# Optimization experiments

Measured on AMD Instinct MI355X. Metric: run time of the kernel, lower is better.

The kernel has to match this reference:

```python
import jax, jax.numpy as jnp
import numpy as np

B, S, HID = 1, 2048, 4096
H, KV, D = 32, 8, 128          # query heads, kv heads, head_dim
THETA = 100000.0               # rope base


def setup_inputs() -> dict:
    key = jax.random.key(0)
    k1, k2, k3, k4, k5 = jax.random.split(key, 5)
    hidden_states = jax.random.normal(k1, (B, S, HID), jnp.float32)
    # W_pack: Linear(hidden, H*D + 2*KV*D), torch weight layout [out, in]
    w_pack = jax.random.normal(k2, (H * D + 2 * KV * D, HID), jnp.float32) * 0.02
    w_o = jax.random.normal(k3, (HID, H * D), jnp.float32) * 0.02
    # conv kernels: per-kv-head causal mixing weights of width 2 (softmax-normalized at init)
    conv_k = jax.nn.softmax(jax.random.normal(k4, (KV, 2), jnp.float32), axis=-1)
    conv_v = jax.nn.softmax(jax.random.normal(k5, (KV, 2), jnp.float32), axis=-1)
    return dict(hidden_states=hidden_states, w_pack=w_pack, w_o=w_o,
                conv_k=conv_k, conv_v=conv_v)


def _causal_conv2(u, k):
    """u: [b,s,h,d], k: [h,2]. v[t] = k[h,0]*u[t-1] + k[h,1]*u[t] (zero pad at t=-1).
    Equivalent to custom_convolution with window 2 (unfold+mul+sum)."""
    prev = jnp.pad(u, ((0, 0), (1, 0), (0, 0), (0, 0)))[:, :-1]
    return k[None, None, :, 0:1] * prev + k[None, None, :, 1:2] * u


def _rope(x):
    """Non-interleaved (half-split) rotary over full head_dim. x: [b,s,h,d]."""
    s, d = x.shape[1], x.shape[-1]
    inv = 1.0 / (THETA ** (jnp.arange(0, d, 2, dtype=jnp.float32) / d))
    freqs = jnp.arange(s, dtype=jnp.float32)[:, None] * inv[None, :]  # [s, d/2]
    cos = jnp.cos(freqs)[None, :, None, :]
    sin = jnp.sin(freqs)[None, :, None, :]
    x1, x2 = x[..., : d // 2], x[..., d // 2:]
    return jnp.concatenate([x1 * cos - x2 * sin, x1 * sin + x2 * cos], axis=-1)


def reference(hidden_states, w_pack, w_o, conv_k, conv_v):
    qkv = hidden_states @ w_pack.T                       # [b,s,H*D+2*KV*D]
    q = qkv[..., : H * D].reshape(B, S, H, D)
    k = qkv[..., H * D: H * D + KV * D].reshape(B, S, KV, D)
    v = qkv[..., H * D + KV * D:].reshape(B, S, KV, D)

    # causal depthwise width-2 conv mixing on K and V (prefill path)
    k = _causal_conv2(k, conv_k)
    v = _causal_conv2(v, conv_v)

    # rotary on q, k
    q = _rope(q)
    k = _rope(k)

    # GQA: repeat kv heads to match query heads
    g = H // KV
    k = jnp.repeat(k, g, axis=2)
    v = jnp.repeat(v, g, axis=2)

    scale = 1.0 / np.sqrt(D).astype(np.float32)
    scores = jnp.einsum('bqhd,bkhd->bhqk', q, k) * scale  # [b,H,S,S]
    causal = jnp.tril(jnp.ones((S, S), dtype=bool))
    scores = jnp.where(causal[None, None], scores, jnp.finfo(scores.dtype).min)
    probs = jax.nn.softmax(scores, axis=-1)
    out = jnp.einsum('bhqk,bkhd->bqhd', probs, v).reshape(B, S, H * D)
    return out @ w_o.T
```

## Files before the change

### kernel.cpp

```cpp
#include <hip/hip_runtime.h>
#include <hip/hip_bf16.h>

#define S_LEN 2048
#define HID 4096
#define NH 32
#define NKV 8
#define HD 128

typedef unsigned short u16;
typedef __attribute__((ext_vector_type(4))) float f32x4;
typedef __attribute__((ext_vector_type(8))) short bf16x8;

__device__ __forceinline__ u16 f2bf(float x) {
  union { float f; unsigned u; } c; c.f = x;
  unsigned r = c.u + 0x7FFFu + ((c.u >> 16) & 1u);
  return (u16)(r >> 16);
}

__device__ __forceinline__ void gload16(const void* g, void* l) {
  __builtin_amdgcn_global_load_lds(
      (const __attribute__((address_space(1))) unsigned int*)g,
      (__attribute__((address_space(3))) unsigned int*)l, 16, 0, 0);
}

__global__ void cvt4_kernel(const float* __restrict__ s, u16* __restrict__ d, int n4) {
  int i = blockIdx.x * 256 + threadIdx.x;
  if (i >= n4) return;
  float4 v = ((const float4*)s)[i];
  ushort4 o;
  o.x = f2bf(v.x); o.y = f2bf(v.y); o.z = f2bf(v.z); o.w = f2bf(v.w);
  ((ushort4*)d)[i] = o;
}

__global__ void rope_tab_kernel(float2* __restrict__ tab) {
  int i = blockIdx.x * 256 + threadIdx.x;
  int t = i >> 6, d = i & 63;
  float inv = expf(-(float)d * (11.512925464970229f / 64.0f));
  float f = (float)t * inv;
  float2 cs; cs.x = cosf(f); cs.y = sinf(f);
  tab[i] = cs;
}

__global__ void rope_q_kernel(const float* __restrict__ qkv, const float2* __restrict__ tab,
                              u16* __restrict__ Q) {
  int i = blockIdx.x * 256 + threadIdx.x;
  int d = i & 63, h = (i >> 6) & 31, t = i >> 11;
  const float* row = qkv + (size_t)t * 6144 + h * 128;
  float x1 = row[d], x2 = row[d + 64];
  float2 cs = tab[(t << 6) | d];
  const float SC = 0.12752551286084f;
  u16* orow = Q + (((size_t)t * NH + h) << 7);
  orow[d]      = f2bf((x1 * cs.x - x2 * cs.y) * SC);
  orow[d + 64] = f2bf((x1 * cs.y + x2 * cs.x) * SC);
}

__global__ void convrope_k_kernel(const float* __restrict__ qkv, const float* __restrict__ ck,
                                  const float2* __restrict__ tab, u16* __restrict__ K) {
  int i = blockIdx.x * 256 + threadIdx.x;
  int d = i & 63, kv = (i >> 6) & 7, t = i >> 9;
  const float* cur = qkv + (size_t)t * 6144 + 4096 + kv * 128;
  float c0 = ck[kv * 2], c1 = ck[kv * 2 + 1];
  float x1 = c1 * cur[d], x2 = c1 * cur[d + 64];
  if (t > 0) { const float* prv = cur - 6144; x1 += c0 * prv[d]; x2 += c0 * prv[d + 64]; }
  float2 cs = tab[(t << 6) | d];
  u16* orow = K + (((size_t)t * NKV + kv) << 7);
  orow[d]      = f2bf(x1 * cs.x - x2 * cs.y);
  orow[d + 64] = f2bf(x1 * cs.y + x2 * cs.x);
}

__global__ __launch_bounds__(256) void convT_v_kernel(const float* __restrict__ qkv,
                                                      const float* __restrict__ cv,
                                                      u16* __restrict__ VT) {
  __shared__ float ld[65][128];
  int tt = blockIdx.x * 64, kv = blockIdx.y;
  float c0 = cv[kv * 2], c1 = cv[kv * 2 + 1];
  for (int idx = threadIdx.x; idx < 65 * 128; idx += 256) {
    int r = idx >> 7, d = idx & 127;
    int t = tt - 1 + r;
    ld[r][d] = (t >= 0) ? qkv[(size_t)t * 6144 + 5120 + kv * 128 + d] : 0.f;
  }
  __syncthreads();
  int d = threadIdx.x >> 1, tc = (threadIdx.x & 1) * 32;
  u16* out = VT + ((size_t)kv * 128 + d) * S_LEN + tt + tc;
#pragma unroll
  for (int j = 0; j < 32; ++j)
    out[j] = f2bf(c0 * ld[tc + j][d] + c1 * ld[tc + j + 1][d]);
}

#define BM 128
#define BN 128
#define BK 64

__global__ __launch_bounds__(256, 2) void gemm_nt_kernel(const u16* __restrict__ A,
                                                         const u16* __restrict__ B,
                                                         float* __restrict__ C,
                                                         int M, int N, int K) {
  __shared__ __align__(16) u16 lA[BM * BK];
  __shared__ __align__(16) u16 lB[BN * BK];
  const int tid = threadIdx.x;
  const int wid = tid >> 6, lane = tid & 63;
  const int bm = blockIdx.y * BM, bn = blockIdx.x * BN;
  const int wr = (wid >> 1) * 64, wc = (wid & 1) * 64;
  const int lr = lane & 15, lg = lane >> 4;
  f32x4 acc[4][4] = {};
  const char* Ab = (const char*)A;
  const char* Bb = (const char*)B;
  const int nk = K / BK;
  for (int kt = 0; kt < nk; ++kt) {
    const size_t k0b = (size_t)kt * (BK * 2);
    __syncthreads();
#pragma unroll
    for (int i = 0; i < 4; ++i) {
      int off = (i * 4 + wid) * 1024 + lane * 16;
      int row = off >> 7, inrow = off & 127;
      int sw = inrow ^ ((row & 7) << 4);
      gload16(Ab + (size_t)(bm + row) * (K * 2) + k0b + sw, (char*)lA + (i * 4 + wid) * 1024);
      gload16(Bb + (size_t)(bn + row) * (K * 2) + k0b + sw, (char*)lB + (i * 4 + wid) * 1024);
    }
    __syncthreads();
    bf16x8 af[4][2], bfv[4][2];
#pragma unroll
    for (int m = 0; m < 4; ++m)
#pragma unroll
      for (int ks = 0; ks < 2; ++ks) {
        int row = wr + m * 16 + lr;
        int boff = row * 128 + ((ks * 64 + lg * 16) ^ ((row & 7) << 4));
        af[m][ks] = *(const bf16x8*)((const char*)lA + boff);
      }
#pragma unroll
    for (int n = 0; n < 4; ++n)
#pragma unroll
      for (int ks = 0; ks < 2; ++ks) {
        int row = wc + n * 16 + lr;
        int boff = row * 128 + ((ks * 64 + lg * 16) ^ ((row & 7) << 4));
        bfv[n][ks] = *(const bf16x8*)((const char*)lB + boff);
      }
#pragma unroll
    for (int m = 0; m < 4; ++m)
#pragma unroll
      for (int n = 0; n < 4; ++n)
#pragma unroll
        for (int ks = 0; ks < 2; ++ks)
          acc[m][n] = __builtin_amdgcn_mfma_f32_16x16x32_bf16(af[m][ks], bfv[n][ks], acc[m][n], 0, 0, 0);
  }
#pragma unroll
  for (int m = 0; m < 4; ++m)
#pragma unroll
    for (int n = 0; n < 4; ++n)
#pragma unroll
      for (int r = 0; r < 4; ++r) {
        int row = bm + wr + m * 16 + lg * 4 + r;
        int col = bn + wc + n * 16 + lr;
        C[(size_t)row * N + col] = acc[m][n][r];
      }
}

__global__ __launch_bounds__(256, 2) void attn_kernel(const u16* __restrict__ Q,
                                                      const u16* __restrict__ K,
                                                      const u16* __restrict__ VT,
                                                      u16* __restrict__ O) {
  __shared__ __align__(16) u16 lK[2][64 * 128];
  __shared__ __align__(16) u16 lV[2][128 * 64];
  __shared__ __align__(16) u16 lP[4][16 * 64];
  const int tid = threadIdx.x;
  const int wid = tid >> 6, lane = tid & 63;
  const int lr = lane & 15, lg = lane >> 4;
  const int q0 = blockIdx.x, h = blockIdx.y;
  const int kvh = h >> 2;
  const int qtA = q0, qtB = 31 - q0;

  bf16x8 qfA[4], qfB[4];
  {
    const int rA = qtA * 64 + wid * 16 + lr;
    const int rB = qtB * 64 + wid * 16 + lr;
#pragma unroll
    for (int ks = 0; ks < 4; ++ks) {
      qfA[ks] = *(const bf16x8*)(Q + (((size_t)rA * NH + h) << 7) + ks * 32 + lg * 8);
      qfB[ks] = *(const bf16x8*)(Q + (((size_t)rB * NH + h) << 7) + ks * 32 + lg * 8);
    }
  }

  f32x4 oA[8] = {}, oB[8] = {};
  float mA[4], lsA[4], mB[4], lsB[4];
#pragma unroll
  for (int r = 0; r < 4; ++r) { mA[r] = mB[r] = -1e30f; lsA[r] = lsB[r] = 0.f; }

  const char* Kb = (const char*)K;
  const char* Vb = (const char*)VT;
  char* pb = (char*)lP[wid];

  auto stage = [&](int buf, int kt) {
    char* dK = (char*)lK[buf];
    char* dV = (char*)lV[buf];
#pragma unroll
    for (int i = 0; i < 4; ++i) {
      int off = (i * 4 + wid) * 1024 + lane * 16;
      int t = off >> 8, inrow = off & 255;
      gload16(Kb + (((size_t)((kt * 64 + t) * NKV + kvh)) << 8) + (inrow ^ ((t & 7) << 4)),
              dK + (i * 4 + wid) * 1024);
      int d = off >> 7, inr2 = off & 127;
      gload16(Vb + ((size_t)(kvh * 128 + d)) * (S_LEN * 2) + kt * 128 + (inr2 ^ ((d & 7) << 4)),
              dV + (i * 4 + wid) * 1024);
    }
  };

  auto step = [&](const bf16x8* qf, f32x4* o, float* mrow, float* lrow, int buf, bool diag) {
    const char* kb = (const char*)lK[buf];
    const char* vb = (const char*)lV[buf];
    f32x4 sv[4];
#pragma unroll
    for (int n = 0; n < 4; ++n) {
      f32x4 a = {};
#pragma unroll
      for (int ks = 0; ks < 4; ++ks) {
        int trow = n * 16 + lr;
        int boff = trow * 256 + ((ks * 64 + lg * 16) ^ ((trow & 7) << 4));
        bf16x8 kf = *(const bf16x8*)(kb + boff);
        a = __builtin_amdgcn_mfma_f32_16x16x32_bf16(qf[ks], kf, a, 0, 0, 0);
      }
      sv[n] = a;
    }
    if (diag) {
#pragma unroll
      for (int n = 0; n < 4; ++n)
#pragma unroll
        for (int r = 0; r < 4; ++r) {
          int col = n * 16 + lr, rw = wid * 16 + lg * 4 + r;
          if (col > rw) sv[n][r] = -1e30f;
        }
    }
    float pm[4];
#pragma unroll
    for (int r = 0; r < 4; ++r)
      pm[r] = fmaxf(fmaxf(sv[0][r], sv[1][r]), fmaxf(sv[2][r], sv[3][r]));
#pragma unroll
    for (int r = 0; r < 4; ++r) {
      pm[r] = fmaxf(pm[r], __shfl_xor(pm[r], 1));
      pm[r] = fmaxf(pm[r], __shfl_xor(pm[r], 2));
      pm[r] = fmaxf(pm[r], __shfl_xor(pm[r], 4));
      pm[r] = fmaxf(pm[r], __shfl_xor(pm[r], 8));
    }
    bool need = (pm[0] > mrow[0] + 8.f) | (pm[1] > mrow[1] + 8.f) |
                (pm[2] > mrow[2] + 8.f) | (pm[3] > mrow[3] + 8.f);
    if (__any(need)) {
#pragma unroll
      for (int r = 0; r < 4; ++r) {
        float mn = fmaxf(mrow[r], pm[r]);
        float al = exp2f(mrow[r] - mn);
        mrow[r] = mn;
        lrow[r] *= al;
#pragma unroll
        for (int nt = 0; nt < 8; ++nt) o[nt][r] *= al;
      }
    }
    float rs[4] = {0.f, 0.f, 0.f, 0.f};
#pragma unroll
    for (int n = 0; n < 4; ++n)
#pragma unroll
      for (int r = 0; r < 4; ++r) {
        float p = exp2f(sv[n][r] - mrow[r]);
        rs[r] += p;
        int row = lg * 4 + r, col = n * 16 + lr;
        int boff = (row * 128 + col * 2) ^ ((row & 7) << 4);
        *(u16*)(pb + boff) = f2bf(p);
      }
#pragma unroll
    for (int r = 0; r < 4; ++r) {
      rs[r] += __shfl_xor(rs[r], 1);
      rs[r] += __shfl_xor(rs[r], 2);
      rs[r] += __shfl_xor(rs[r], 4);
      rs[r] += __shfl_xor(rs[r], 8);
      lrow[r] += rs[r];
    }
#pragma unroll
    for (int ks = 0; ks < 2; ++ks) {
      int aboff = lr * 128 + ((ks * 64 + lg * 16) ^ ((lr & 7) << 4));
      bf16x8 pf = *(const bf16x8*)(pb + aboff);
#pragma unroll
      for (int nt = 0; nt < 8; ++nt) {
        int drow = nt * 16 + lr;
        int vboff = drow * 128 + ((ks * 64 + lg * 16) ^ ((drow & 7) << 4));
        bf16x8 vf = *(const bf16x8*)(vb + vboff);
        o[nt] = __builtin_amdgcn_mfma_f32_16x16x32_bf16(pf, vf, o[nt], 0, 0, 0);
      }
    }
  };

  stage(0, 0);
  __syncthreads();
  for (int kt = 0; kt <= qtB; ++kt) {
    int cur = kt & 1;
    if (kt < qtB) stage(cur ^ 1, kt + 1);
    if (kt <= qtA) step(qfA, oA, mA, lsA, cur, kt == qtA);
    step(qfB, oB, mB, lsB, cur, kt == qtB);
    __syncthreads();
  }

#pragma unroll
  for (int r = 0; r < 4; ++r) { lsA[r] = 1.0f / lsA[r]; lsB[r] = 1.0f / lsB[r]; }
#pragma unroll
  for (int nt = 0; nt < 8; ++nt)
#pragma unroll
    for (int r = 0; r < 4; ++r) {
      int rowA = qtA * 64 + wid * 16 + lg * 4 + r;
      int rowB = qtB * 64 + wid * 16 + lg * 4 + r;
      int col = nt * 16 + lr;
      O[(size_t)rowA * 4096 + h * 128 + col] = f2bf(oA[nt][r] * lsA[r]);
      O[(size_t)rowB * 4096 + h * 128 + col] = f2bf(oB[nt][r] * lsB[r]);
    }
}

extern "C" void kernel_launch(void* const* d_in, const int* in_sizes, int n_in,
                              void* d_out, int out_size, void* d_ws, size_t ws_size,
                              hipStream_t stream) {
  const float* hidden = (const float*)d_in[0];
  const float* wpack  = (const float*)d_in[1];
  const float* wo     = (const float*)d_in[2];
  const float* convk  = (const float*)d_in[3];
  const float* convv  = (const float*)d_in[4];
  float* out = (float*)d_out;

  char* w = (char*)d_ws;
  u16*  hiddenB = (u16*)w;
  u16*  wpackB  = (u16*)(w + 16777216);
  float* qkv    = (float*)(w + 67108864);
  u16*  qrope   = (u16*)(w + 117440512);
  u16*  krope   = (u16*)(w + 134217728);
  u16*  vT      = (u16*)(w + 138412032);
  float2* tab   = (float2*)(w + 142606336);

  cvt4_kernel<<<8192, 256, 0, stream>>>(hidden, hiddenB, 2097152);
  cvt4_kernel<<<24576, 256, 0, stream>>>(wpack, wpackB, 6291456);
  rope_tab_kernel<<<512, 256, 0, stream>>>(tab);
  gemm_nt_kernel<<<dim3(48, 16), 256, 0, stream>>>(hiddenB, wpackB, qkv, 2048, 6144, 4096);
  cvt4_kernel<<<16384, 256, 0, stream>>>(wo, wpackB, 4194304);
  rope_q_kernel<<<16384, 256, 0, stream>>>(qkv, tab, qrope);
  convrope_k_kernel<<<4096, 256, 0, stream>>>(qkv, convk, tab, krope);
  convT_v_kernel<<<dim3(32, 8), 256, 0, stream>>>(qkv, convv, vT);
  attn_kernel<<<dim3(16, 32), 256, 0, stream>>>(qrope, krope, vT, hiddenB);
  gemm_nt_kernel<<<dim3(32, 16), 256, 0, stream>>>(hiddenB, wpackB, out, 2048, 4096, 4096);
}
```

Before: 530.2 us.

## Split attention q-tiles across wave pairs and remap GEMM blocks per XCD

In the attention kernel, each wave used to process 16 rows of both the low and high q-tile. Now two waves own the low tile and two own the high tile, 32 rows each. This shares each K/V fragment load across two MFMAs and removes the serialized A and B steps per wave. The GEMM kernel also remaps block IDs so consecutive tiles land on the same XCD for better L2 locality. The cost is load imbalance: waves on the short tile sit idle while the long tile finishes, and the larger P buffer raises LDS use and register pressure.

```diff
diff --git a/kernel.cpp b/kernel.cpp
--- a/kernel.cpp
+++ b/kernel.cpp
@@ -99,7 +99,11 @@
   __shared__ __align__(16) u16 lB[BN * BK];
   const int tid = threadIdx.x;
   const int wid = tid >> 6, lane = tid & 63;
-  const int bm = blockIdx.y * BM, bn = blockIdx.x * BN;
+  const int nbx = gridDim.x, nwg = nbx * gridDim.y;
+  const int L = blockIdx.y * nbx + blockIdx.x;
+  const int cpx = nwg >> 3;
+  const int W = (L & 7) * cpx + (L >> 3);
+  const int bm = (W / nbx) * BM, bn = (W % nbx) * BN;
   const int wr = (wid >> 1) * 64, wc = (wid & 1) * 64;
   const int lr = lane & 15, lg = lane >> 4;
   f32x4 acc[4][4] = {};
@@ -161,29 +165,30 @@
                                                       u16* __restrict__ O) {
   __shared__ __align__(16) u16 lK[2][64 * 128];
   __shared__ __align__(16) u16 lV[2][128 * 64];
-  __shared__ __align__(16) u16 lP[4][16 * 64];
+  __shared__ __align__(16) u16 lP[4][32 * 64];
   const int tid = threadIdx.x;
   const int wid = tid >> 6, lane = tid & 63;
   const int lr = lane & 15, lg = lane >> 4;
   const int q0 = blockIdx.x, h = blockIdx.y;
   const int kvh = h >> 2;
   const int qtA = q0, qtB = 31 - q0;
-
-  bf16x8 qfA[4], qfB[4];
-  {
-    const int rA = qtA * 64 + wid * 16 + lr;
-    const int rB = qtB * 64 + wid * 16 + lr;
-#pragma unroll
-    for (int ks = 0; ks < 4; ++ks) {
-      qfA[ks] = *(const bf16x8*)(Q + (((size_t)rA * NH + h) << 7) + ks * 32 + lg * 8);
-      qfB[ks] = *(const bf16x8*)(Q + (((size_t)rB * NH + h) << 7) + ks * 32 + lg * 8);
-    }
-  }
-
-  f32x4 oA[8] = {}, oB[8] = {};
-  float mA[4], lsA[4], mB[4], lsB[4];
-#pragma unroll
-  for (int r = 0; r < 4; ++r) { mA[r] = mB[r] = -1e30f; lsA[r] = lsB[r] = 0.f; }
+  const int tile = wid >> 1, w2 = wid & 1;
+  const int qt = tile ? qtB : qtA;
+  const int qbase = qt * 64 + w2 * 32;
+
+  bf16x8 qf[2][4];
+#pragma unroll
+  for (int m = 0; m < 2; ++m)
+#pragma unroll
+    for (int ks = 0; ks < 4; ++ks)
+      qf[m][ks] = *(const bf16x8*)(Q + (((size_t)(qbase + m * 16 + lr) * NH + h) << 7) + ks * 32 + lg * 8);
+
+  f32x4 o[2][8] = {};
+  float mrow[2][4], lrow[2][4];
+#pragma unroll
+  for (int m = 0; m < 2; ++m)
+#pragma unroll
+    for (int r = 0; r < 4; ++r) { mrow[m][r] = -1e30f; lrow[m][r] = 0.f; }
 
   const char* Kb = (const char*)K;
   const char* Vb = (const char*)VT;
@@ -204,84 +209,101 @@
     }
   };
 
-  auto step = [&](const bf16x8* qf, f32x4* o, float* mrow, float* lrow, int buf, bool diag) {
+  auto step = [&](int buf, bool diag) {
     const char* kb = (const char*)lK[buf];
     const char* vb = (const char*)lV[buf];
-    f32x4 sv[4];
-#pragma unroll
-    for (int n = 0; n < 4; ++n) {
-      f32x4 a = {};
+    f32x4 sv[2][4] = {};
+#pragma unroll
+    for (int n = 0; n < 4; ++n)
 #pragma unroll
       for (int ks = 0; ks < 4; ++ks) {
         int trow = n * 16 + lr;
         int boff = trow * 256 + ((ks * 64 + lg * 16) ^ ((trow & 7) << 4));
         bf16x8 kf = *(const bf16x8*)(kb + boff);
-        a = __builtin_amdgcn_mfma_f32_16x16x32_bf16(qf[ks], kf, a, 0, 0, 0);
-      }
-      sv[n] = a;
-    }
+        sv[0][n] = __builtin_amdgcn_mfma_f32_16x16x32_bf16(qf[0][ks], kf, sv[0][n], 0, 0, 0);
+        sv[1][n] = __builtin_amdgcn_mfma_f32_16x16x32_bf16(qf[1][ks], kf, sv[1][n], 0, 0, 0);
+      }
     if (diag) {
 #pragma unroll
+      for (int m = 0; m < 2; ++m)
+#pragma unroll
+        for (int n = 0; n < 4; ++n)
+#pragma unroll
+          for (int r = 0; r < 4; ++r) {
+            int col = n * 16 + lr, rw = w2 * 32 + m * 16 + lg * 4 + r;
+            if (col > rw) sv[m][n][r] = -1e30f;
+          }
+    }
+    float pm[2][4];
+#pragma unroll
+    for (int m = 0; m < 2; ++m)
+#pragma unroll
+      for (int r = 0; r < 4; ++r) {
+        float v = fmaxf(fmaxf(sv[m][0][r], sv[m][1][r]), fmaxf(sv[m][2][r], sv[m][3][r]));
+        v = fmaxf(v, __shfl_xor(v, 1));
+        v = fmaxf(v, __shfl_xor(v, 2));
+        v = fmaxf(v, __shfl_xor(v, 4));
+        v = fmaxf(v, __shfl_xor(v, 8));
+        pm[m][r] = v;
+      }
+    bool need = false;
+#pragma unroll
+    for (int m = 0; m < 2; ++m)
+#pragma unroll
+      for (int r = 0; r < 4; ++r)
+        need |= (pm[m][r] > mrow[m][r] + 8.f);
+    if (__any(need)) {
+#pragma unroll
+      for (int m = 0; m < 2; ++m)
+#pragma unroll
+        for (int r = 0; r < 4; ++r) {
+          float mn = fmaxf(mrow[m][r], pm[m][r]);
+          float al = exp2f(mrow[m][r] - mn);
+          mrow[m][r] = mn;
+          lrow[m][r] *= al;
+#pragma unroll
+          for (int nt = 0; nt < 8; ++nt) o[m][nt][r] *= al;
+        }
+    }
+#pragma unroll
+    for (int m = 0; m < 2; ++m) {
+      float rs[4] = {0.f, 0.f, 0.f, 0.f};
+#pragma unroll
       for (int n = 0; n < 4; ++n)
 #pragma unroll
         for (int r = 0; r < 4; ++r) {
-          int col = n * 16 + lr, rw = wid * 16 + lg * 4 + r;
-          if (col > rw) sv[n][r] = -1e30f;
+          float p = exp2f(sv[m][n][r] - mrow[m][r]);
+          rs[r] += p;
+          int row = m * 16 + lg * 4 + r, col = n * 16 + lr;
+          int boff = (row * 128 + col * 2) ^ ((row & 7) << 4);
+          *(u16*)(pb + boff) = f2bf(p);
         }
-    }
-    float pm[4];
-#pragma unroll
-    for (int r = 0; r < 4; ++r)
-      pm[r] = fmaxf(fmaxf(sv[0][r], sv[1][r]), fmaxf(sv[2][r], sv[3][r]));
-#pragma unroll
-    for (int r = 0; r < 4; ++r) {
-      pm[r] = fmaxf(pm[r], __shfl_xor(pm[r], 1));
-      pm[r] = fmaxf(pm[r], __shfl_xor(pm[r], 2));
-      pm[r] = fmaxf(pm[r], __shfl_xor(pm[r], 4));
-      pm[r] = fmaxf(pm[r], __shfl_xor(pm[r], 8));
-    }
-    bool need = (pm[0] > mrow[0] + 8.f) | (pm[1] > mrow[1] + 8.f) |
-                (pm[2] > mrow[2] + 8.f) | (pm[3] > mrow[3] + 8.f);
-    if (__any(need)) {
 #pragma unroll
       for (int r = 0; r < 4; ++r) {
-        float mn = fmaxf(mrow[r], pm[r]);
-        float al = exp2f(mrow[r] - mn);
-        mrow[r] = mn;
-        lrow[r] *= al;
-#pragma unroll
-        for (int nt = 0; nt < 8; ++nt) o[nt][r] *= al;
-      }
-    }
-    float rs[4] = {0.f, 0.f, 0.f, 0.f};
-#pragma unroll
-    for (int n = 0; n < 4; ++n)
-#pragma unroll
-      for (int r = 0; r < 4; ++r) {
-        float p = exp2f(sv[n][r] - mrow[r]);
-        rs[r] += p;
-        int row = lg * 4 + r, col = n * 16 + lr;
-        int boff = (row * 128 + col * 2) ^ ((row & 7) << 4);
-        *(u16*)(pb + boff) = f2bf(p);
-      }
-#pragma unroll
-    for (int r = 0; r < 4; ++r) {
-      rs[r] += __shfl_xor(rs[r], 1);
-      rs[r] += __shfl_xor(rs[r], 2);
-      rs[r] += __shfl_xor(rs[r], 4);
-      rs[r] += __shfl_xor(rs[r], 8);
-      lrow[r] += rs[r];
+        float v = rs[r];
+        v += __shfl_xor(v, 1);
+        v += __shfl_xor(v, 2);
+        v += __shfl_xor(v, 4);
+        v += __shfl_xor(v, 8);
+        lrow[m][r] += v;
+      }
     }
 #pragma unroll
     for (int ks = 0; ks < 2; ++ks) {
-      int aboff = lr * 128 + ((ks * 64 + lg * 16) ^ ((lr & 7) << 4));
-      bf16x8 pf = *(const bf16x8*)(pb + aboff);
+      bf16x8 pf[2];
+#pragma unroll
+      for (int m = 0; m < 2; ++m) {
+        int prow = m * 16 + lr;
+        int aboff = prow * 128 + ((ks * 64 + lg * 16) ^ ((prow & 7) << 4));
+        pf[m] = *(const bf16x8*)(pb + aboff);
+      }
 #pragma unroll
       for (int nt = 0; nt < 8; ++nt) {
         int drow = nt * 16 + lr;
         int vboff = drow * 128 + ((ks * 64 + lg * 16) ^ ((drow & 7) << 4));
         bf16x8 vf = *(const bf16x8*)(vb + vboff);
-        o[nt] = __builtin_amdgcn_mfma_f32_16x16x32_bf16(pf, vf, o[nt], 0, 0, 0);
+        o[0][nt] = __builtin_amdgcn_mfma_f32_16x16x32_bf16(pf[0], vf, o[0][nt], 0, 0, 0);
+        o[1][nt] = __builtin_amdgcn_mfma_f32_16x16x32_bf16(pf[1], vf, o[1][nt], 0, 0, 0);
       }
     }
   };
@@ -291,23 +313,24 @@
   for (int kt = 0; kt <= qtB; ++kt) {
     int cur = kt & 1;
     if (kt < qtB) stage(cur ^ 1, kt + 1);
-    if (kt <= qtA) step(qfA, oA, mA, lsA, cur, kt == qtA);
-    step(qfB, oB, mB, lsB, cur, kt == qtB);
+    if (kt <= qt) step(cur, kt == qt);
     __syncthreads();
   }
 
 #pragma unroll
-  for (int r = 0; r < 4; ++r) { lsA[r] = 1.0f / lsA[r]; lsB[r] = 1.0f / lsB[r]; }
-#pragma unroll
-  for (int nt = 0; nt < 8; ++nt)
-#pragma unroll
-    for (int r = 0; r < 4; ++r) {
-      int rowA = qtA * 64 + wid * 16 + lg * 4 + r;
-      int rowB = qtB * 64 + wid * 16 + lg * 4 + r;
-      int col = nt * 16 + lr;
-      O[(size_t)rowA * 4096 + h * 128 + col] = f2bf(oA[nt][r] * lsA[r]);
-      O[(size_t)rowB * 4096 + h * 128 + col] = f2bf(oB[nt][r] * lsB[r]);
-    }
+  for (int m = 0; m < 2; ++m)
+#pragma unroll
+    for (int r = 0; r < 4; ++r) lrow[m][r] = 1.0f / lrow[m][r];
+#pragma unroll
+  for (int m = 0; m < 2; ++m)
+#pragma unroll
+    for (int nt = 0; nt < 8; ++nt)
+#pragma unroll
+      for (int r = 0; r < 4; ++r) {
+        int row = qbase + m * 16 + lg * 4 + r;
+        int col = nt * 16 + lr;
+        O[(size_t)row * 4096 + h * 128 + col] = f2bf(o[m][nt][r] * lrow[m][r]);
+      }
 }
 
 extern "C" void kernel_launch(void* const* d_in, const int* in_sizes, int n_in,
```

New measurement: 555.0 us. 1.05x slower.

## Restructure attention to pair adjacent q-tiles, transpose QK^T, remap GEMM blocks across XCDs

Applied to the files above, without the earlier changes.

Each attention block now handles two adjacent query tiles (2b, 2b+1) instead of a head/tail pair. Work is ordered heaviest-first, and heads sharing a KV group are placed close together in the grid. QK^T is computed transposed so each lane owns one query row, which turns the row max and sum into two cross-lane shuffles. Packed bf16 conversion writes P to LDS, and the K/V fragment loads are shared between both tiles' MFMAs. GEMM workgroups are remapped so consecutive tiles land on the same XCD for L2 reuse. The cost is that paired adjacent tiles lose the balanced causal workload of the old head/tail pairing, and there are extra ds_bpermute broadcasts for rescaling.

```diff
diff --git a/kernel.cpp b/kernel.cpp
--- a/kernel.cpp
+++ b/kernel.cpp
@@ -21,6 +21,17 @@
   __builtin_amdgcn_global_load_lds(
       (const __attribute__((address_space(1))) unsigned int*)g,
       (__attribute__((address_space(3))) unsigned int*)l, 16, 0, 0);
+}
+
+__device__ __forceinline__ unsigned cvtpk_bf16(float lo, float hi) {
+  unsigned r;
+  asm("v_cvt_pk_bf16_f32 %0, %1, %2" : "=v"(r) : "v"(lo), "v"(hi));
+  return r;
+}
+
+__device__ __forceinline__ float bcastf(float v, int srclane) {
+  int r = __builtin_amdgcn_ds_bpermute(srclane << 2, __builtin_bit_cast(int, v));
+  return __builtin_bit_cast(float, r);
 }
 
 __global__ void cvt4_kernel(const float* __restrict__ s, u16* __restrict__ d, int n4) {
@@ -99,7 +110,11 @@
   __shared__ __align__(16) u16 lB[BN * BK];
   const int tid = threadIdx.x;
   const int wid = tid >> 6, lane = tid & 63;
-  const int bm = blockIdx.y * BM, bn = blockIdx.x * BN;
+  const int nbx = gridDim.x, nwg = nbx * gridDim.y;
+  const int L = blockIdx.y * nbx + blockIdx.x;
+  const int cpx = nwg >> 3;
+  const int W = (L & 7) * cpx + (L >> 3);
+  const int bm = (W / nbx) * BM, bn = (W % nbx) * BN;
   const int wr = (wid >> 1) * 64, wc = (wid & 1) * 64;
   const int lr = lane & 15, lg = lane >> 4;
   f32x4 acc[4][4] = {};
@@ -161,33 +176,33 @@
                                                       u16* __restrict__ O) {
   __shared__ __align__(16) u16 lK[2][64 * 128];
   __shared__ __align__(16) u16 lV[2][128 * 64];
-  __shared__ __align__(16) u16 lP[4][16 * 64];
+  __shared__ __align__(16) u16 lP[4][2][16 * 64];
   const int tid = threadIdx.x;
   const int wid = tid >> 6, lane = tid & 63;
   const int lr = lane & 15, lg = lane >> 4;
-  const int q0 = blockIdx.x, h = blockIdx.y;
+  const int g = blockIdx.x;
+  const int s = g & 255;
+  const int h = s >> 3, j = s & 7;
+  const int b = (g < 256) ? (15 - j) : j;
   const int kvh = h >> 2;
-  const int qtA = q0, qtB = 31 - q0;
+  const int qtA = 2 * b, qtB = 2 * b + 1;
+  const int qrowA = qtA * 64 + wid * 16 + lr;
+  const int qrowB = qtB * 64 + wid * 16 + lr;
 
   bf16x8 qfA[4], qfB[4];
-  {
-    const int rA = qtA * 64 + wid * 16 + lr;
-    const int rB = qtB * 64 + wid * 16 + lr;
-#pragma unroll
-    for (int ks = 0; ks < 4; ++ks) {
-      qfA[ks] = *(const bf16x8*)(Q + (((size_t)rA * NH + h) << 7) + ks * 32 + lg * 8);
-      qfB[ks] = *(const bf16x8*)(Q + (((size_t)rB * NH + h) << 7) + ks * 32 + lg * 8);
-    }
+#pragma unroll
+  for (int ks = 0; ks < 4; ++ks) {
+    qfA[ks] = *(const bf16x8*)(Q + (((size_t)qrowA * NH + h) << 7) + ks * 32 + lg * 8);
+    qfB[ks] = *(const bf16x8*)(Q + (((size_t)qrowB * NH + h) << 7) + ks * 32 + lg * 8);
   }
 
   f32x4 oA[8] = {}, oB[8] = {};
-  float mA[4], lsA[4], mB[4], lsB[4];
-#pragma unroll
-  for (int r = 0; r < 4; ++r) { mA[r] = mB[r] = -1e30f; lsA[r] = lsB[r] = 0.f; }
+  float mA = -1e30f, sumA = 0.f, mB = -1e30f, sumB = 0.f;
 
   const char* Kb = (const char*)K;
   const char* Vb = (const char*)VT;
-  char* pb = (char*)lP[wid];
+  char* pbA = (char*)lP[wid][0];
+  char* pbB = (char*)lP[wid][1];
 
   auto stage = [&](int buf, int kt) {
     char* dK = (char*)lK[buf];
@@ -204,85 +219,54 @@
     }
   };
 
-  auto step = [&](const bf16x8* qf, f32x4* o, float* mrow, float* lrow, int buf, bool diag) {
-    const char* kb = (const char*)lK[buf];
-    const char* vb = (const char*)lV[buf];
-    f32x4 sv[4];
+  auto smx = [&](f32x4* sv, float& mm, float& ll, f32x4* o, char* pbuf, bool diag, int qrow, int kt) {
+    if (diag) {
+#pragma unroll
+      for (int n = 0; n < 4; ++n)
+#pragma unroll
+        for (int r = 0; r < 4; ++r) {
+          int kg = kt * 64 + n * 16 + lg * 4 + r;
+          if (kg > qrow) sv[n][r] = -1e30f;
+        }
+    }
+    float pm = sv[0][0];
+#pragma unroll
+    for (int n = 0; n < 4; ++n)
+#pragma unroll
+      for (int r = 0; r < 4; ++r) pm = fmaxf(pm, sv[n][r]);
+    pm = fmaxf(pm, __shfl_xor(pm, 16));
+    pm = fmaxf(pm, __shfl_xor(pm, 32));
+    if (__any(pm > mm + 8.f)) {
+      float mn = fmaxf(mm, pm);
+      float al = exp2f(mm - mn);
+      mm = mn;
+      ll *= al;
+      float alo[4];
+#pragma unroll
+      for (int r = 0; r < 4; ++r) alo[r] = bcastf(al, lg * 4 + r);
+#pragma unroll
+      for (int nt = 0; nt < 8; ++nt)
+#pragma unroll
+        for (int r = 0; r < 4; ++r) o[nt][r] *= alo[r];
+    }
+    float rs = 0.f;
+#pragma unroll
+    for (int n = 0; n < 4; ++n)
+#pragma unroll
+      for (int r = 0; r < 4; ++r) {
+        float p = exp2f(sv[n][r] - mm);
+        sv[n][r] = p;
+        rs += p;
+      }
+    rs += __shfl_xor(rs, 16);
+    rs += __shfl_xor(rs, 32);
+    ll += rs;
 #pragma unroll
     for (int n = 0; n < 4; ++n) {
-      f32x4 a = {};
-#pragma unroll
-      for (int ks = 0; ks < 4; ++ks) {
-        int trow = n * 16 + lr;
-        int boff = trow * 256 + ((ks * 64 + lg * 16) ^ ((trow & 7) << 4));
-        bf16x8 kf = *(const bf16x8*)(kb + boff);
-        a = __builtin_amdgcn_mfma_f32_16x16x32_bf16(qf[ks], kf, a, 0, 0, 0);
-      }
-      sv[n] = a;
-    }
-    if (diag) {
-#pragma unroll
-      for (int n = 0; n < 4; ++n)
-#pragma unroll
-        for (int r = 0; r < 4; ++r) {
-          int col = n * 16 + lr, rw = wid * 16 + lg * 4 + r;
-          if (col > rw) sv[n][r] = -1e30f;
-        }
-    }
-    float pm[4];
-#pragma unroll
-    for (int r = 0; r < 4; ++r)
-      pm[r] = fmaxf(fmaxf(sv[0][r], sv[1][r]), fmaxf(sv[2][r], sv[3][r]));
-#pragma unroll
-    for (int r = 0; r < 4; ++r) {
-      pm[r] = fmaxf(pm[r], __shfl_xor(pm[r], 1));
-      pm[r] = fmaxf(pm[r], __shfl_xor(pm[r], 2));
-      pm[r] = fmaxf(pm[r], __shfl_xor(pm[r], 4));
-      pm[r] = fmaxf(pm[r], __shfl_xor(pm[r], 8));
-    }
-    bool need = (pm[0] > mrow[0] + 8.f) | (pm[1] > mrow[1] + 8.f) |
-                (pm[2] > mrow[2] + 8.f) | (pm[3] > mrow[3] + 8.f);
-    if (__any(need)) {
-#pragma unroll
-      for (int r = 0; r < 4; ++r) {
-        float mn = fmaxf(mrow[r], pm[r]);
-        float al = exp2f(mrow[r] - mn);
-        mrow[r] = mn;
-        lrow[r] *= al;
-#pragma unroll
-        for (int nt = 0; nt < 8; ++nt) o[nt][r] *= al;
-      }
-    }
-    float rs[4] = {0.f, 0.f, 0.f, 0.f};
-#pragma unroll
-    for (int n = 0; n < 4; ++n)
-#pragma unroll
-      for (int r = 0; r < 4; ++r) {
-        float p = exp2f(sv[n][r] - mrow[r]);
-        rs[r] += p;
-        int row = lg * 4 + r, col = n * 16 + lr;
-        int boff = (row * 128 + col * 2) ^ ((row & 7) << 4);
-        *(u16*)(pb + boff) = f2bf(p);
-      }
-#pragma unroll
-    for (int r = 0; r < 4; ++r) {
-      rs[r] += __shfl_xor(rs[r], 1);
-      rs[r] += __shfl_xor(rs[r], 2);
-      rs[r] += __shfl_xor(rs[r], 4);
-      rs[r] += __shfl_xor(rs[r], 8);
-      lrow[r] += rs[r];
-    }
-#pragma unroll
-    for (int ks = 0; ks < 2; ++ks) {
-      int aboff = lr * 128 + ((ks * 64 + lg * 16) ^ ((lr & 7) << 4));
-      bf16x8 pf = *(const bf16x8*)(pb + aboff);
-#pragma unroll
-      for (int nt = 0; nt < 8; ++nt) {
-        int drow = nt * 16 + lr;
-        int vboff = drow * 128 + ((ks * 64 + lg * 16) ^ ((drow & 7) << 4));
-        bf16x8 vf = *(const bf16x8*)(vb + vboff);
-        o[nt] = __builtin_amdgcn_mfma_f32_16x16x32_bf16(pf, vf, o[nt], 0, 0, 0);
-      }
+      uint2 w;
+      w.x = cvtpk_bf16(sv[n][0], sv[n][1]);
+      w.y = cvtpk_bf16(sv[n][2], sv[n][3]);
+      *(uint2*)(pbuf + ((lr * 128 + n * 32 + lg * 8) ^ ((lr & 7) << 4))) = w;
     }
   };
 
@@ -291,13 +275,52 @@
   for (int kt = 0; kt <= qtB; ++kt) {
     int cur = kt & 1;
     if (kt < qtB) stage(cur ^ 1, kt + 1);
-    if (kt <= qtA) step(qfA, oA, mA, lsA, cur, kt == qtA);
-    step(qfB, oB, mB, lsB, cur, kt == qtB);
+    const char* kb = (const char*)lK[cur];
+    const char* vb = (const char*)lV[cur];
+    const bool doA = (kt <= qtA);
+
+    f32x4 svA[4], svB[4];
+#pragma unroll
+    for (int n = 0; n < 4; ++n) {
+      f32x4 aA = {}, aB = {};
+#pragma unroll
+      for (int ks = 0; ks < 4; ++ks) {
+        int trow = n * 16 + lr;
+        int boff = trow * 256 + ((ks * 64 + lg * 16) ^ ((trow & 7) << 4));
+        bf16x8 kf = *(const bf16x8*)(kb + boff);
+        aB = __builtin_amdgcn_mfma_f32_16x16x32_bf16(kf, qfB[ks], aB, 0, 0, 0);
+        aA = __builtin_amdgcn_mfma_f32_16x16x32_bf16(kf, qfA[ks], aA, 0, 0, 0);
+      }
+      svA[n] = aA; svB[n] = aB;
+    }
+
+    if (doA) smx(svA, mA, sumA, oA, pbA, kt == qtA, qrowA, kt);
+    smx(svB, mB, sumB, oB, pbB, kt == qtB, qrowB, kt);
+
+#pragma unroll
+    for (int ks = 0; ks < 2; ++ks) {
+      int poff = (lr * 128 + 64 * ks + 16 * lg) ^ ((lr & 7) << 4);
+      bf16x8 pfB = *(const bf16x8*)(pbB + poff);
+      bf16x8 pfA = *(const bf16x8*)(pbA + poff);
+#pragma unroll
+      for (int nt = 0; nt < 8; ++nt) {
+        int drow = nt * 16 + lr;
+        int vboff = drow * 128 + ((ks * 64 + lg * 16) ^ ((drow & 7) << 4));
+        bf16x8 vf = *(const bf16x8*)(vb + vboff);
+        oB[nt] = __builtin_amdgcn_mfma_f32_16x16x32_bf16(pfB, vf, oB[nt], 0, 0, 0);
+        if (doA) oA[nt] = __builtin_amdgcn_mfma_f32_16x16x32_bf16(pfA, vf, oA[nt], 0, 0, 0);
+      }
+    }
     __syncthreads();
   }
 
-#pragma unroll
-  for (int r = 0; r < 4; ++r) { lsA[r] = 1.0f / lsA[r]; lsB[r] = 1.0f / lsB[r]; }
+  float riA = 1.0f / sumA, riB = 1.0f / sumB;
+  float rA[4], rB[4];
+#pragma unroll
+  for (int r = 0; r < 4; ++r) {
+    rA[r] = bcastf(riA, lg * 4 + r);
+    rB[r] = bcastf(riB, lg * 4 + r);
+  }
 #pragma unroll
   for (int nt = 0; nt < 8; ++nt)
 #pragma unroll
@@ -305,8 +328,8 @@
       int rowA = qtA * 64 + wid * 16 + lg * 4 + r;
       int rowB = qtB * 64 + wid * 16 + lg * 4 + r;
       int col = nt * 16 + lr;
-      O[(size_t)rowA * 4096 + h * 128 + col] = f2bf(oA[nt][r] * lsA[r]);
-      O[(size_t)rowB * 4096 + h * 128 + col] = f2bf(oB[nt][r] * lsB[r]);
+      O[(size_t)rowA * 4096 + h * 128 + col] = f2bf(oA[nt][r] * rA[r]);
+      O[(size_t)rowB * 4096 + h * 128 + col] = f2bf(oB[nt][r] * rB[r]);
     }
 }
 
@@ -337,6 +360,6 @@
   rope_q_kernel<<<16384, 256, 0, stream>>>(qkv, tab, qrope);
   convrope_k_kernel<<<4096, 256, 0, stream>>>(qkv, convk, tab, krope);
   convT_v_kernel<<<dim3(32, 8), 256, 0, stream>>>(qkv, convv, vT);
-  attn_kernel<<<dim3(16, 32), 256, 0, stream>>>(qrope, krope, vT, hiddenB);
+  attn_kernel<<<512, 256, 0, stream>>>(qrope, krope, vT, hiddenB);
   gemm_nt_kernel<<<dim3(32, 16), 256, 0, stream>>>(hiddenB, wpackB, out, 2048, 4096, 4096);
 }
```

Measured after the change: 529.7 us. Within noise of the previous version (-0.1%).
